# Kernel tuning notes

Hardware: AMD Instinct MI355X
Metric: run time of the kernel (lower is better)

## Reference

```python
import jax, jax.numpy as jnp
import numpy as np

M, N, K = 1024, 11008, 4096


def _unpack_i2u(Bp):
    """Unpack 2-bit unsigned weights per decode_i2u_to_i8s interleave.

    Bp: [N, K//4] int8 storage. Within each group of 4 bytes (16 elements),
    output element at position 4*i + j = (byte_j >> (2*i)) & 3.
    Returns [N, K] int8 with values in {0,1,2,3}.
    """
    Bu = jax.lax.bitcast_convert_type(Bp, jnp.uint8)  # [N, K//4]
    n, kc = Bu.shape
    Bg = Bu.reshape(n, kc // 4, 1, 4)                 # [N, G, 1, j]
    shifts = (jnp.arange(4, dtype=jnp.uint8) * jnp.uint8(2)).reshape(1, 1, 4, 1)
    vals = (Bg >> shifts) & jnp.uint8(3)              # [N, G, i, j]
    return vals.reshape(n, kc * 4).astype(jnp.int8)   # [N, K]


def setup_inputs() -> dict:
    key = jax.random.key(0)
    k1, k2 = jax.random.split(key)
    A = jax.random.randint(k1, (M, K), -128, 128, dtype=jnp.int8)
    B = jax.random.randint(k2, (N, K // 4), -128, 128, dtype=jnp.int8)
    return {"A": A, "B": B}


def reference(A, B):
    W = _unpack_i2u(B)  # [N, K] int8
    C = jax.lax.dot_general(
        A, W,
        dimension_numbers=(((1,), (1,)), ((), ())),
        preferred_element_type=jnp.int32,
    )  # [M, N] int32
    return C
```

## Files before the change

kernel.cpp:

```cpp
#include <hip/hip_runtime.h>
#include <stdint.h>


#define MM 1024
#define NN 11008
#define KK 4096
#define MTILES 8
#define NTILES 86
#define NBLOCKS (MTILES * NTILES)
#define STRIDE_A ((size_t)MTILES * 8192)
#define STRIDE_B ((size_t)NTILES * 2048)

using i32x4  = __attribute__((ext_vector_type(4))) int;
using i32x16 = __attribute__((ext_vector_type(16))) int;

__device__ __forceinline__ int pack4(i32x4 v) {
    return (int)(((uint32_t)v[0] & 0xFFu) | (((uint32_t)v[1] & 0xFFu) << 8)
               | (((uint32_t)v[2] & 0xFFu) << 16) | (((uint32_t)v[3] & 0xFFu) << 24));
}

__global__ __launch_bounds__(256) void prep_AB(const int* __restrict__ Asrc,
                                               const int* __restrict__ Bsrc,
                                               uint8_t* __restrict__ A2,
                                               uint8_t* __restrict__ B3) {
    if (blockIdx.x < 1024) {
        const int g = blockIdx.x * 256 + threadIdx.x;
        const int kstep = g >> 12;
        const int rem   = g & 4095;
        const int mtile = rem >> 9;
        const int c     = rem & 511;
        const int row32 = (c >> 7) & 3, kk2 = (c >> 6) & 1;
        const int lane  = c & 63;
        const int row   = mtile * 128 + row32 * 32 + (lane & 31);
        const int kbyte = kstep * 64 + kk2 * 32 + (lane >> 5) * 16;
        const i32x4* s4 = (const i32x4*)(Asrc + (size_t)row * KK + kbyte);
        i32x4 o;
#pragma unroll
        for (int q = 0; q < 4; ++q) o[q] = pack4(s4[q]);
        *(i32x4*)(A2 + (size_t)g * 16) = o;
    } else {
        const int t = (blockIdx.x - 1024) * 256 + threadIdx.x;
        const int n = t >> 6, kstep = t & 63;
        const int ntile = n >> 7, hf = (n >> 6) & 1, ni = (n >> 5) & 1, l31 = n & 31;
        const i32x4* s4 = (const i32x4*)(Bsrc + (size_t)n * (KK / 4) + kstep * 16);
        int w[4];
#pragma unroll
        for (int j = 0; j < 4; ++j) w[j] = pack4(s4[j]);
        uint8_t* base = B3 + ((size_t)kstep * NTILES + ntile) * 2048 + hf * 1024;
        *(int2*)(base + l31 * 16 + ni * 8)        = make_int2(w[0], w[2]);
        *(int2*)(base + (l31 + 32) * 16 + ni * 8) = make_int2(w[1], w[3]);
    }
}

#define GLOAD_LDS16(g, l) __builtin_amdgcn_global_load_lds(                    \
        (const __attribute__((address_space(1))) uint32_t*)(g),                \
        (__attribute__((address_space(3))) uint32_t*)(l), 16, 0, 0)

#define MFMA_I8 __builtin_amdgcn_mfma_i32_32x32x32_i8

#define STAGE2(SL, T2) do {                                                    \
    const uint8_t* s0_ = gA + (size_t)(2 * (T2)) * STRIDE_A;                   \
    const uint8_t* s1_ = s0_ + STRIDE_A;                                       \
    uint8_t* l_ = &As[SL][0];                                                  \
    GLOAD_LDS16(s0_,        l_ + wave * 1024);                                 \
    GLOAD_LDS16(s0_ + 4096, l_ + 4096 + wave * 1024);                          \
    GLOAD_LDS16(s1_,        l_ + 8192 + wave * 1024);                          \
    GLOAD_LDS16(s1_ + 4096, l_ + 12288 + wave * 1024);                         \
} while (0)

#define BLOAD2(BI, T2) do {                                                    \
    bb0[BI] = *(const i32x4*)(gB + (size_t)(2 * (T2)) * STRIDE_B);             \
    bb1[BI] = *(const i32x4*)(gB + (size_t)(2 * (T2) + 1) * STRIDE_B);         \
} while (0)

#define COMP2(SL, BI) do {                                                     \
    _Pragma("unroll")                                                          \
    for (int sub_ = 0; sub_ < 2; ++sub_) {                                     \
        const uint8_t* ab_ = &As[SL][sub_ * 8192];                             \
        const i32x4 bv_ = sub_ ? bb1[BI] : bb0[BI];                            \
        i32x4 aA0_ = *(const i32x4*)(ab_ + (wr * 2 + 0) * 2048 + lane * 16);   \
        i32x4 aA1_ = *(const i32x4*)(ab_ + (wr * 2 + 0) * 2048 + 1024 + lane * 16); \
        i32x4 aB0_ = *(const i32x4*)(ab_ + (wr * 2 + 1) * 2048 + lane * 16);   \
        i32x4 aB1_ = *(const i32x4*)(ab_ + (wr * 2 + 1) * 2048 + 1024 + lane * 16); \
        _Pragma("unroll")                                                      \
        for (int kk2_ = 0; kk2_ < 2; ++kk2_) {                                 \
            const uint32_t q0_ = (uint32_t)bv_[kk2_];                          \
            const uint32_t q1_ = (uint32_t)bv_[2 + kk2_];                      \
            i32x4 b0_, b1_;                                                    \
            _Pragma("unroll")                                                  \
            for (int i_ = 0; i_ < 4; ++i_) {                                   \
                b0_[i_] = (int)((q0_ >> (2 * i_)) & 0x03030303u);              \
                b1_[i_] = (int)((q1_ >> (2 * i_)) & 0x03030303u);              \
            }                                                                  \
            const i32x4 am0_ = kk2_ ? aA1_ : aA0_;                             \
            const i32x4 am1_ = kk2_ ? aB1_ : aB0_;                             \
            acc[0][0] = MFMA_I8(am0_, b0_, acc[0][0], 0, 0, 0);                \
            acc[0][1] = MFMA_I8(am0_, b1_, acc[0][1], 0, 0, 0);                \
            acc[1][0] = MFMA_I8(am1_, b0_, acc[1][0], 0, 0, 0);                \
            acc[1][1] = MFMA_I8(am1_, b1_, acc[1][1], 0, 0, 0);                \
        }                                                                      \
    }                                                                          \
} while (0)

#define ITER2(T, SL, SLN, BI, BN, NW, DS, DB) do {                             \
    asm volatile("s_waitcnt vmcnt(" #NW ")" ::: "memory");                     \
    __builtin_amdgcn_s_barrier();                                              \
    __builtin_amdgcn_sched_barrier(0);                                         \
    if (DB) BLOAD2(BN, (T) + 1);                                               \
    if (DS) STAGE2(SLN, (T) + 2);                                              \
    COMP2(SL, BI);                                                             \
} while (0)

__global__ __launch_bounds__(256, 3) void bitnet_gemm(const uint8_t* __restrict__ A2,
                                                      const uint8_t* __restrict__ B3,
                                                      int* __restrict__ C) {
    const int tid  = threadIdx.x;
    const int lane = tid & 63, wave = tid >> 6;
    const int wr   = wave >> 1, wc = wave & 1;
    const int l31  = lane & 31, h = lane >> 5;

    const int bid = blockIdx.x;
    const int l   = (bid & 7) * (NBLOCKS / 8) + (bid >> 3);
    const int bm  = l & 7;
    const int bn  = l >> 3;

    __shared__ __align__(16) uint8_t As[3][16384];

    const uint8_t* gA = A2 + (size_t)bm * 8192 + tid * 16;
    const uint8_t* gB = B3 + (size_t)bn * 2048 + wc * 1024 + lane * 16;

    i32x16 acc[2][2] = {};
    i32x4 bb0[2], bb1[2];

    BLOAD2(0, 0);
    STAGE2(0, 0);
    STAGE2(1, 1);

#pragma unroll 1
    for (int t = 0; t < 30; t += 6) {
        ITER2(t + 0, 0, 2, 0, 1, 4, 1, 1);
        ITER2(t + 1, 1, 0, 1, 0, 4, 1, 1);
        ITER2(t + 2, 2, 1, 0, 1, 4, 1, 1);
        ITER2(t + 3, 0, 2, 1, 0, 4, 1, 1);
        ITER2(t + 4, 1, 0, 0, 1, 4, 1, 1);
        ITER2(t + 5, 2, 1, 1, 0, 4, 1, 1);
    }
    ITER2(30, 0, 2, 0, 1, 4, 0, 1);
    ITER2(31, 1, 0, 1, 0, 0, 0, 0);

    const int brow = bm * 128, bcol = bn * 128;
#pragma unroll
    for (int mi = 0; mi < 2; ++mi)
#pragma unroll
        for (int ni = 0; ni < 2; ++ni) {
            const int colg = bcol + wc * 64 + ni * 32 + l31;
#pragma unroll
            for (int r = 0; r < 16; ++r) {
                const int rowin = (r & 3) + 8 * (r >> 2) + 4 * h;
                const int rowg  = brow + wr * 64 + mi * 32 + rowin;
                C[(size_t)rowg * NN + colg] = acc[mi][ni][r];
            }
        }
}

extern "C" void kernel_launch(void* const* d_in, const int* in_sizes, int n_in,
                              void* d_out, int out_size, void* d_ws, size_t ws_size,
                              hipStream_t stream) {
    const int* A32 = (const int*)d_in[0];
    const int* B32 = (const int*)d_in[1];
    int* C = (int*)d_out;

    uint8_t* A2 = (uint8_t*)d_ws;
    uint8_t* B3 = A2 + (size_t)MM * KK;

    prep_AB<<<dim3(1024 + 2752), dim3(256), 0, stream>>>(A32, B32, A2, B3);
    bitnet_gemm<<<dim3(NBLOCKS), dim3(256), 0, stream>>>(A2, B3, C);
}
```

Baseline: 66.02 us.

## Split K across wave pairs with LDS reduction instead of splitting N

Changes the per-block wave decomposition from a 2x2 M/N split to a 2-way M split times a 2-way K split. Each wave now covers the full 128-column tile over half of K, which doubles its accumulators to eight 32x32 tiles. The two K halves are combined through an LDS reduction in the epilogue. This makes each A fragment read from LDS feed four MFMAs instead of two, cutting LDS traffic per MFMA. In exchange it raises accumulator register pressure, which threatens the three-blocks-per-CU occupancy, and adds extra barriers and an LDS round trip at the end.

```diff
diff --git a/kernel.cpp b/kernel.cpp
--- a/kernel.cpp
+++ b/kernel.cpp
@@ -59,45 +59,38 @@
 #define MFMA_I8 __builtin_amdgcn_mfma_i32_32x32x32_i8
 
 #define STAGE2(SL, T2) do {                                                    \
-    const uint8_t* s0_ = gA + (size_t)(2 * (T2)) * STRIDE_A;                   \
-    const uint8_t* s1_ = s0_ + STRIDE_A;                                       \
-    uint8_t* l_ = &As[SL][0];                                                  \
-    GLOAD_LDS16(s0_,        l_ + wave * 1024);                                 \
-    GLOAD_LDS16(s0_ + 4096, l_ + 4096 + wave * 1024);                          \
-    GLOAD_LDS16(s1_,        l_ + 8192 + wave * 1024);                          \
-    GLOAD_LDS16(s1_ + 4096, l_ + 12288 + wave * 1024);                         \
+    const uint8_t* s_ = gA + (size_t)(T2) * STRIDE_A;                          \
+    uint8_t* l_ = &As[SL][kh * 8192 + wr * 4096];                              \
+    GLOAD_LDS16(s_,        l_);                                                \
+    GLOAD_LDS16(s_ + 1024, l_ + 1024);                                         \
+    GLOAD_LDS16(s_ + 2048, l_ + 2048);                                         \
+    GLOAD_LDS16(s_ + 3072, l_ + 3072);                                         \
 } while (0)
 
 #define BLOAD2(BI, T2) do {                                                    \
-    bb0[BI] = *(const i32x4*)(gB + (size_t)(2 * (T2)) * STRIDE_B);             \
-    bb1[BI] = *(const i32x4*)(gB + (size_t)(2 * (T2) + 1) * STRIDE_B);         \
+    c0[BI] = *(const i32x4*)(gB + (size_t)(T2) * STRIDE_B);                    \
+    c1[BI] = *(const i32x4*)(gB + (size_t)(T2) * STRIDE_B + 1024);             \
 } while (0)
 
 #define COMP2(SL, BI) do {                                                     \
+    const uint8_t* ab_ = &As[SL][kh * 8192];                                   \
+    i32x4 aA0_ = *(const i32x4*)(ab_ + (wr * 2 + 0) * 2048 + lane * 16);       \
+    i32x4 aA1_ = *(const i32x4*)(ab_ + (wr * 2 + 0) * 2048 + 1024 + lane * 16);\
+    i32x4 aB0_ = *(const i32x4*)(ab_ + (wr * 2 + 1) * 2048 + lane * 16);       \
+    i32x4 aB1_ = *(const i32x4*)(ab_ + (wr * 2 + 1) * 2048 + 1024 + lane * 16);\
     _Pragma("unroll")                                                          \
-    for (int sub_ = 0; sub_ < 2; ++sub_) {                                     \
-        const uint8_t* ab_ = &As[SL][sub_ * 8192];                             \
-        const i32x4 bv_ = sub_ ? bb1[BI] : bb0[BI];                            \
-        i32x4 aA0_ = *(const i32x4*)(ab_ + (wr * 2 + 0) * 2048 + lane * 16);   \
-        i32x4 aA1_ = *(const i32x4*)(ab_ + (wr * 2 + 0) * 2048 + 1024 + lane * 16); \
-        i32x4 aB0_ = *(const i32x4*)(ab_ + (wr * 2 + 1) * 2048 + lane * 16);   \
-        i32x4 aB1_ = *(const i32x4*)(ab_ + (wr * 2 + 1) * 2048 + 1024 + lane * 16); \
+    for (int kk2_ = 0; kk2_ < 2; ++kk2_) {                                     \
+        const i32x4 am0_ = kk2_ ? aA1_ : aA0_;                                 \
+        const i32x4 am1_ = kk2_ ? aB1_ : aB0_;                                 \
         _Pragma("unroll")                                                      \
-        for (int kk2_ = 0; kk2_ < 2; ++kk2_) {                                 \
-            const uint32_t q0_ = (uint32_t)bv_[kk2_];                          \
-            const uint32_t q1_ = (uint32_t)bv_[2 + kk2_];                      \
-            i32x4 b0_, b1_;                                                    \
+        for (int nc_ = 0; nc_ < 4; ++nc_) {                                    \
+            const uint32_t q_ = (uint32_t)((nc_ < 2 ? c0[BI] : c1[BI])[(nc_ & 1) * 2 + kk2_]); \
+            i32x4 b_;                                                          \
             _Pragma("unroll")                                                  \
-            for (int i_ = 0; i_ < 4; ++i_) {                                   \
-                b0_[i_] = (int)((q0_ >> (2 * i_)) & 0x03030303u);              \
-                b1_[i_] = (int)((q1_ >> (2 * i_)) & 0x03030303u);              \
-            }                                                                  \
-            const i32x4 am0_ = kk2_ ? aA1_ : aA0_;                             \
-            const i32x4 am1_ = kk2_ ? aB1_ : aB0_;                             \
-            acc[0][0] = MFMA_I8(am0_, b0_, acc[0][0], 0, 0, 0);                \
-            acc[0][1] = MFMA_I8(am0_, b1_, acc[0][1], 0, 0, 0);                \
-            acc[1][0] = MFMA_I8(am1_, b0_, acc[1][0], 0, 0, 0);                \
-            acc[1][1] = MFMA_I8(am1_, b1_, acc[1][1], 0, 0, 0);                \
+            for (int i_ = 0; i_ < 4; ++i_)                                     \
+                b_[i_] = (int)((q_ >> (2 * i_)) & 0x03030303u);                \
+            acc[0][nc_] = MFMA_I8(am0_, b_, acc[0][nc_], 0, 0, 0);             \
+            acc[1][nc_] = MFMA_I8(am1_, b_, acc[1][nc_], 0, 0, 0);             \
         }                                                                      \
     }                                                                          \
 } while (0)
@@ -116,7 +109,8 @@
                                                       int* __restrict__ C) {
     const int tid  = threadIdx.x;
     const int lane = tid & 63, wave = tid >> 6;
-    const int wr   = wave >> 1, wc = wave & 1;
+    const int wr   = wave >> 1;
+    const int kh   = wave & 1;
     const int l31  = lane & 31, h = lane >> 5;
 
     const int bid = blockIdx.x;
@@ -126,11 +120,13 @@
 
     __shared__ __align__(16) uint8_t As[3][16384];
 
-    const uint8_t* gA = A2 + (size_t)bm * 8192 + tid * 16;
-    const uint8_t* gB = B3 + (size_t)bn * 2048 + wc * 1024 + lane * 16;
-
-    i32x16 acc[2][2] = {};
-    i32x4 bb0[2], bb1[2];
+    const uint8_t* gA = A2 + (size_t)(kh * 32) * STRIDE_A + (size_t)bm * 8192
+                      + wr * 4096 + lane * 16;
+    const uint8_t* gB = B3 + (size_t)(kh * 32) * STRIDE_B + (size_t)bn * 2048
+                      + lane * 16;
+
+    i32x16 acc[2][4] = {};
+    i32x4 c0[2], c1[2];
 
     BLOAD2(0, 0);
     STAGE2(0, 0);
@@ -148,19 +144,49 @@
     ITER2(30, 0, 2, 0, 1, 4, 0, 1);
     ITER2(31, 1, 0, 1, 0, 0, 0, 0);
 
-    const int brow = bm * 128, bcol = bn * 128;
-#pragma unroll
-    for (int mi = 0; mi < 2; ++mi)
-#pragma unroll
-        for (int ni = 0; ni < 2; ++ni) {
-            const int colg = bcol + wc * 64 + ni * 32 + l31;
-#pragma unroll
-            for (int r = 0; r < 16; ++r) {
-                const int rowin = (r & 3) + 8 * (r >> 2) + 4 * h;
-                const int rowg  = brow + wr * 64 + mi * 32 + rowin;
-                C[(size_t)rowg * NN + colg] = acc[mi][ni][r];
-            }
+    i32x4* red = (i32x4*)&As[0][0];
+    const int brow = bm * 128 + wr * 64, bcol = bn * 128;
+#pragma unroll
+    for (int g = 0; g < 2; ++g) {
+        __syncthreads();
+        if (wr == g && kh == 1) {
+#pragma unroll
+            for (int mi = 0; mi < 2; ++mi)
+#pragma unroll
+                for (int nc = 0; nc < 4; ++nc) {
+                    const i32x16 v = acc[mi][nc];
+#pragma unroll
+                    for (int q = 0; q < 4; ++q) {
+                        i32x4 s;
+                        s[0] = v[q * 4 + 0]; s[1] = v[q * 4 + 1];
+                        s[2] = v[q * 4 + 2]; s[3] = v[q * 4 + 3];
+                        red[((mi * 4 + nc) * 4 + q) * 64 + lane] = s;
+                    }
+                }
         }
+        __syncthreads();
+        if (wr == g && kh == 0) {
+#pragma unroll
+            for (int mi = 0; mi < 2; ++mi)
+#pragma unroll
+                for (int nc = 0; nc < 4; ++nc) {
+                    i32x16 v = acc[mi][nc];
+#pragma unroll
+                    for (int q = 0; q < 4; ++q) {
+                        const i32x4 r = red[((mi * 4 + nc) * 4 + q) * 64 + lane];
+                        v[q * 4 + 0] += r[0]; v[q * 4 + 1] += r[1];
+                        v[q * 4 + 2] += r[2]; v[q * 4 + 3] += r[3];
+                    }
+                    const int colg = bcol + nc * 32 + l31;
+#pragma unroll
+                    for (int r = 0; r < 16; ++r) {
+                        const int rowin = (r & 3) + 8 * (r >> 2) + 4 * h;
+                        const int rowg  = brow + mi * 32 + rowin;
+                        C[(size_t)rowg * NN + colg] = v[r];
+                    }
+                }
+        }
+    }
 }
 
 extern "C" void kernel_launch(void* const* d_in, const int* in_sizes, int n_in,
```

Measured after the change: 74.32 us. +12.6%, slower.
